# Kernel optimization log

Measured on AMD Instinct MI355X. Metric: run time of the kernel, lower is better.

Reference implementation:

```python
import jax, jax.numpy as jnp
import numpy as np

B, CL, H, W, NP = 128, 8, 16, 16, 32   # batch, primary cap length, height, width, n primary capsules
NC, CLO, ITER = 10, 16, 3              # n output capsules, output capsule length, routing iterations


def squash(t):
    # TensorMONK Activations 'squash': squash along axis 2 of a 3D tensor
    ss = jnp.sum(t * t, axis=2, keepdims=True)
    return (ss / (1.0 + ss)) * t / jnp.sqrt(ss)


def setup_inputs() -> dict:
    key = jax.random.key(0)
    k1, k2 = jax.random.split(key)
    tensor = jax.random.normal(k1, (B, CL, H, W, NP), dtype=jnp.float32)
    # nn.Parameter(torch.randn(...).normal_(0.0, 0.1)) -> N(0, 0.1)
    weight = 0.1 * jax.random.normal(k2, (CL * H * W, NP, NC * CLO), dtype=jnp.float32)
    return {"tensor": tensor, "weight": weight}


def reference(tensor, weight):
    b, cl, h, w, n_prim = tensor.shape
    # flatten spatial/length dims, squash along primary-capsule axis (dim 2, faithful to source)
    x = squash(tensor.reshape(b, -1, n_prim))                  # (B, P, N) with P = cl*h*w
    # (B,P,1,N) @ (P,N,K) broadcasted matmul -> (B,P,K)
    u = jnp.einsum('bpn,pnk->bpk', x, weight)
    u = u.reshape(b, cl, h, w, NC, CLO)                        # (B, cl, h, w, NC, CLO)
    bias = jnp.zeros((b, cl, h, w, NC), dtype=tensor.dtype)
    v = None
    for i in range(ITER):  # fixed small iteration count
        c = jax.nn.softmax(bias, axis=4)                       # softmax over output capsules
        s = jnp.einsum('bchwn,bchwnk->bnk', c, u)              # weighted sum over cl,h,w
        v = squash(s)                                          # squash along capsule length (axis 2)
        if i < ITER - 1:
            bias = bias + jnp.einsum('bchwnk,bnk->bchwn', u, v)
    return v
```

## Files before the change

### kernel.cpp

```cpp
#include <hip/hip_runtime.h>

typedef unsigned short u16;
typedef __attribute__((ext_vector_type(8))) short bf16x8;
typedef __attribute__((ext_vector_type(4))) float f32x4;

#define B_   128
#define P_   2048
#define NC_  10
#define F_   160
#define NBLK 512
#define PPB  4
#define NTHR 512
#define XS   40
#define WS   40

__device__ __forceinline__ u16 f2bf(float f) {
    union { float f; unsigned u; } v; v.f = f;
    unsigned r = v.u + 0x7FFFu + ((v.u >> 16) & 1u);
    return (u16)(r >> 16);
}
__device__ __forceinline__ float bf2f(u16 h) {
    union { unsigned u; float f; } v; v.u = ((unsigned)h) << 16;
    return v.f;
}

__global__ void k_squash_x(const float* __restrict__ t, u16* __restrict__ xb) {
    int g = blockIdx.x * 256 + threadIdx.x;
    int pair = g >> 2, sub = g & 3;
    int p = pair & 2047, b = pair >> 11;
    const float4* tg = (const float4*)t;
    int fi = pair * 8 + sub * 2;
    float4 va = tg[fi], vb = tg[fi + 1];
    float ss = va.x*va.x + va.y*va.y + va.z*va.z + va.w*va.w
             + vb.x*vb.x + vb.y*vb.y + vb.z*vb.z + vb.w*vb.w;
    ss += __shfl_xor(ss, 1);
    ss += __shfl_xor(ss, 2);
    float fct = ss / ((1.f + ss) * sqrtf(ss));
    u16 h[8] __attribute__((aligned(16)));
    h[0]=f2bf(va.x*fct); h[1]=f2bf(va.y*fct); h[2]=f2bf(va.z*fct); h[3]=f2bf(va.w*fct);
    h[4]=f2bf(vb.x*fct); h[5]=f2bf(vb.y*fct); h[6]=f2bf(vb.z*fct); h[7]=f2bf(vb.w*fct);
    *(uint4*)(xb + (p * 128 + b) * 32 + sub * 8) = *(const uint4*)h;
}

__global__ void k_wt(const float* __restrict__ w, u16* __restrict__ wb) {
    __shared__ u16 wl[32 * F_];
    int p = blockIdx.x, tid = threadIdx.x;
    const float4* wp = (const float4*)(w + p * 32 * F_);
    for (int e4 = tid; e4 < 1280; e4 += 256) {
        float4 v = wp[e4];
        u16 h[4] __attribute__((aligned(8)));
        h[0]=f2bf(v.x); h[1]=f2bf(v.y); h[2]=f2bf(v.z); h[3]=f2bf(v.w);
        *(ushort4*)(wl + e4 * 4) = *(const ushort4*)h;
    }
    __syncthreads();
    u16* wo = wb + p * F_ * 32;
    for (int sid = tid; sid < 640; sid += 256) {
        int f = sid >> 2, k0 = (sid & 3) << 3;
        u16 tmp[8] __attribute__((aligned(16)));
#pragma unroll
        for (int j = 0; j < 8; ++j) tmp[j] = wl[(k0 + j) * F_ + f];
        *(uint4*)(wo + f * 32 + k0) = *(const uint4*)tmp;
    }
}

template<int MODE>
__global__ __launch_bounds__(NTHR, 2) void k_pass(
        const u16* __restrict__ xb, const u16* __restrict__ wb,
        const float* __restrict__ vprev, u16* __restrict__ s_part)
{
    __shared__ u16 xt[128 * XS];
    __shared__ u16 wt[F_ * WS];
    const int tid = threadIdx.x, blk = blockIdx.x;
    const int L = tid & 63, wv = tid >> 6;
    const int q = L >> 4, col = L & 15;
    const int b = wv * 16 + col;
    const int p0 = blk * PPB;

    float4 vv[NC_];
    if (MODE != 0) {
#pragma unroll
        for (int n = 0; n < NC_; ++n)
            vv[n] = *(const float4*)(vprev + b * F_ + n * 16 + q * 4);
    }

    f32x4 s_acc[NC_];
#pragma unroll
    for (int n = 0; n < NC_; ++n) s_acc[n] = (f32x4){0.f, 0.f, 0.f, 0.f};

    uint4 r0, r1, r2;
    {
        const uint4* xg = (const uint4*)(xb + p0 * 4096);
        const uint4* wg = (const uint4*)(wb + p0 * 5120);
        r0 = xg[tid]; r1 = wg[tid];
        if (tid < 128) r2 = wg[tid + 512];
    }

#pragma unroll
    for (int pp = 0; pp < PPB; ++pp) {
        __syncthreads();
        *(uint4*)&xt[(tid >> 2) * XS + (tid & 3) * 8] = r0;
        *(uint4*)&wt[(tid >> 2) * WS + (tid & 3) * 8] = r1;
        if (tid < 128)
            *(uint4*)&wt[(128 + (tid >> 2)) * WS + (tid & 3) * 8] = r2;
        if (pp + 1 < PPB) {
            const uint4* xg = (const uint4*)(xb + (p0 + pp + 1) * 4096);
            const uint4* wg = (const uint4*)(wb + (p0 + pp + 1) * 5120);
            r0 = xg[tid]; r1 = wg[tid];
            if (tid < 128) r2 = wg[tid + 512];
        }
        __syncthreads();

        bf16x8 bfrag = *(const bf16x8*)&xt[b * XS + q * 8];
        if (MODE == 0) {
#pragma unroll
            for (int n = 0; n < NC_; ++n) {
                bf16x8 afrag = *(const bf16x8*)&wt[(n * 16 + col) * WS + q * 8];
                s_acc[n] = __builtin_amdgcn_mfma_f32_16x16x32_bf16(afrag, bfrag, s_acc[n], 0, 0, 0);
            }
        } else {
            float tt[NC_];
#pragma unroll
            for (int n = 0; n < NC_; ++n) {
                bf16x8 afrag = *(const bf16x8*)&wt[(n * 16 + col) * WS + q * 8];
                f32x4 z = {0.f, 0.f, 0.f, 0.f};
                f32x4 acc = __builtin_amdgcn_mfma_f32_16x16x32_bf16(afrag, bfrag, z, 0, 0, 0);
                float t = acc[0]*vv[n].x + acc[1]*vv[n].y + acc[2]*vv[n].z + acc[3]*vv[n].w;
                t += __shfl_xor(t, 16);
                t += __shfl_xor(t, 32);
                tt[n] = t;
            }
            float mx = tt[0];
#pragma unroll
            for (int n = 1; n < NC_; ++n) mx = fmaxf(mx, tt[n]);
            float den = 0.f;
#pragma unroll
            for (int n = 0; n < NC_; ++n) { tt[n] = __expf(tt[n] - mx); den += tt[n]; }
            float inv = 1.f / den;
#pragma unroll
            for (int n = 0; n < NC_; ++n) {
                bf16x8 afrag = *(const bf16x8*)&wt[(n * 16 + col) * WS + q * 8];
                f32x4 z = {0.f, 0.f, 0.f, 0.f};
                f32x4 acc = __builtin_amdgcn_mfma_f32_16x16x32_bf16(afrag, bfrag, z, 0, 0, 0);
                float cf = tt[n] * inv;
#pragma unroll
                for (int r = 0; r < 4; ++r) s_acc[n][r] += cf * acc[r];
            }
        }
    }

    u16* sp = s_part + blk * (B_ * F_);
    const float sc = (MODE == 0) ? 0.1f : 1.f;
#pragma unroll
    for (int n = 0; n < NC_; ++n) {
        u16 h[4] __attribute__((aligned(8)));
#pragma unroll
        for (int r = 0; r < 4; ++r) h[r] = f2bf(s_acc[n][r] * sc);
        *(ushort4*)(sp + b * F_ + n * 16 + q * 4) = *(const ushort4*)h;
    }
}

template<int ADD>
__global__ void k_red(const u16* __restrict__ s_part,
                      const float* __restrict__ vprev, float* __restrict__ vout) {
    __shared__ float r0s[256], r1s[256];
    const int tid = threadIdx.x, blk = blockIdx.x;
    const int pid = tid & 31, part = tid >> 5;
    const uint* sp = (const uint*)s_part;
    const int opair = blk * 32 + pid;
    float a0 = 0.f, a1 = 0.f;
#pragma unroll 8
    for (int g = part; g < NBLK; g += 8) {
        uint u = sp[g * 10240 + opair];
        a0 += bf2f((u16)(u & 0xffff));
        a1 += bf2f((u16)(u >> 16));
    }
    r0s[tid] = a0; r1s[tid] = a1;
    __syncthreads();
    if (tid < 32) {
        float s0 = 0.f, s1 = 0.f;
#pragma unroll
        for (int k = 0; k < 8; ++k) { s0 += r0s[k * 32 + tid]; s1 += r1s[k * 32 + tid]; }
        float sq = s0 * s0 + s1 * s1;
        sq += __shfl_xor(sq, 1);
        sq += __shfl_xor(sq, 2);
        sq += __shfl_xor(sq, 4);
        float fct = sq / ((1.f + sq) * sqrtf(sq));
        float2 o = make_float2(s0 * fct, s1 * fct);
        if (ADD) {
            float2 pv = *(const float2*)(vprev + 2 * (blk * 32 + tid));
            o.x += pv.x; o.y += pv.y;
        }
        *(float2*)(vout + 2 * (blk * 32 + tid)) = o;
    }
}

extern "C" void kernel_launch(void* const* d_in, const int* in_sizes, int n_in,
                              void* d_out, int out_size, void* d_ws, size_t ws_size,
                              hipStream_t stream) {
    const float* tensor = (const float*)d_in[0];
    const float* weight = (const float*)d_in[1];
    float* out = (float*)d_out;
    char* ws = (char*)d_ws;

    u16*   xb     = (u16*)(ws);
    u16*   wb     = (u16*)(ws + 16777216);
    u16*   s_part = (u16*)(ws + 37748736);
    float* v0     = (float*)(ws + 58720256);
    float* vs     = (float*)(ws + 58802176);

    k_squash_x<<<4096, 256, 0, stream>>>(tensor, xb);
    k_wt<<<2048, 256, 0, stream>>>(weight, wb);

    k_pass<0><<<NBLK, NTHR, 0, stream>>>(xb, wb, nullptr, s_part);
    k_red<0><<<320, 256, 0, stream>>>(s_part, nullptr, v0);
    k_pass<1><<<NBLK, NTHR, 0, stream>>>(xb, wb, v0, s_part);
    k_red<1><<<320, 256, 0, stream>>>(s_part, v0, vs);
    k_pass<2><<<NBLK, NTHR, 0, stream>>>(xb, wb, vs, s_part);
    k_red<0><<<320, 256, 0, stream>>>(s_part, nullptr, out);
}
```

Before: 174.1 us.

## Fuse routing passes into one cooperative kernel with LDS-resident tiles

Replaces the three pass kernels and three reduce kernels with a single cooperative kernel. Each of 256 blocks loads its 8 primary positions of x and W into shared memory once, then reuses them across all routing iterations, with grid.sync between the partial-sum and reduction phases. It also XOR-swizzles the bf16 layouts of x and W to cut LDS bank conflicts, and computes u once per position instead of running the MFMA twice in routing iterations. The cost is about 150 KB of LDS per block, which limits occupancy to one block per CU, plus grid-wide barriers. The previous multi-kernel path is kept as a fallback if the cooperative launch fails.

```diff
diff --git a/kernel.cpp b/kernel.cpp
--- a/kernel.cpp
+++ b/kernel.cpp
@@ -1,18 +1,25 @@
 #include <hip/hip_runtime.h>
+#include <hip/hip_cooperative_groups.h>
+
+namespace cg = cooperative_groups;
 
 typedef unsigned short u16;
+typedef unsigned int u32;
 typedef __attribute__((ext_vector_type(8))) short bf16x8;
 typedef __attribute__((ext_vector_type(4))) float f32x4;
 
-#define B_   128
-#define P_   2048
-#define NC_  10
-#define F_   160
-#define NBLK 512
-#define PPB  4
-#define NTHR 512
-#define XS   40
-#define WS   40
+#define B_    128
+#define P_    2048
+#define NC_   10
+#define F_    160
+#define NTHR  512
+
+#define CBLK  256
+#define CPPB  8
+
+#define GBLK  512
+#define XS    40
+#define WS    40
 
 __device__ __forceinline__ u16 f2bf(float f) {
     union { float f; unsigned u; } v; v.f = f;
@@ -39,7 +46,8 @@
     u16 h[8] __attribute__((aligned(16)));
     h[0]=f2bf(va.x*fct); h[1]=f2bf(va.y*fct); h[2]=f2bf(va.z*fct); h[3]=f2bf(va.w*fct);
     h[4]=f2bf(vb.x*fct); h[5]=f2bf(vb.y*fct); h[6]=f2bf(vb.z*fct); h[7]=f2bf(vb.w*fct);
-    *(uint4*)(xb + (p * 128 + b) * 32 + sub * 8) = *(const uint4*)h;
+    int sw = sub ^ ((b >> 1) & 3);
+    *(uint4*)(xb + (p * 128 + b) * 32 + sw * 8) = *(const uint4*)h;
 }
 
 __global__ void k_wt(const float* __restrict__ w, u16* __restrict__ wb) {
@@ -59,7 +67,160 @@
         u16 tmp[8] __attribute__((aligned(16)));
 #pragma unroll
         for (int j = 0; j < 8; ++j) tmp[j] = wl[(k0 + j) * F_ + f];
-        *(uint4*)(wo + f * 32 + k0) = *(const uint4*)tmp;
+        int sw = (sid & 3) ^ ((f >> 1) & 3);
+        *(uint4*)(wo + f * 32 + sw * 8) = *(const uint4*)tmp;
+    }
+}
+
+__global__ __launch_bounds__(NTHR, 2) void k_route(
+        const u16* __restrict__ xb, const u16* __restrict__ wb,
+        u16* __restrict__ s_part, float* __restrict__ v0,
+        float* __restrict__ vs, float* __restrict__ out)
+{
+    __shared__ u16 xt[CPPB * 128 * 32];
+    __shared__ u16 wt[CPPB * 160 * 32];
+    __shared__ float red[2 * NTHR];
+
+    const int tid = threadIdx.x, blk = blockIdx.x;
+    const int L = tid & 63, wv = tid >> 6;
+    const int q = L >> 4, col = L & 15;
+    const int b = wv * 16 + col;
+    const int qs = (q ^ ((col >> 1) & 3)) * 8;
+    const int p0 = blk * CPPB;
+
+    {
+        const uint4* xg = (const uint4*)(xb + (size_t)p0 * 4096);
+        const uint4* wg = (const uint4*)(wb + (size_t)p0 * 5120);
+        uint4 rx[8], rw[10];
+#pragma unroll
+        for (int i = 0; i < 8; ++i)  rx[i] = xg[i * NTHR + tid];
+#pragma unroll
+        for (int i = 0; i < 10; ++i) rw[i] = wg[i * NTHR + tid];
+        uint4* xl = (uint4*)xt; uint4* wl4 = (uint4*)wt;
+#pragma unroll
+        for (int i = 0; i < 8; ++i)  xl[i * NTHR + tid] = rx[i];
+#pragma unroll
+        for (int i = 0; i < 10; ++i) wl4[i * NTHR + tid] = rw[i];
+    }
+    __syncthreads();
+
+    cg::grid_group grid = cg::this_grid();
+
+    for (int itn = 0; itn < 3; ++itn) {
+        f32x4 s_acc[NC_];
+#pragma unroll
+        for (int n = 0; n < NC_; ++n) s_acc[n] = (f32x4){0.f, 0.f, 0.f, 0.f};
+
+        if (itn == 0) {
+            for (int pp = 0; pp < CPPB; ++pp) {
+                bf16x8 bfrag = *(const bf16x8*)&xt[(pp * 128 + b) * 32 + qs];
+#pragma unroll
+                for (int n = 0; n < NC_; ++n) {
+                    bf16x8 afrag = *(const bf16x8*)&wt[(pp * 160 + n * 16 + col) * 32 + qs];
+                    s_acc[n] = __builtin_amdgcn_mfma_f32_16x16x32_bf16(afrag, bfrag, s_acc[n], 0, 0, 0);
+                }
+            }
+        } else {
+            const float* vp = (itn == 1) ? v0 : vs;
+            float4 vv[NC_];
+#pragma unroll
+            for (int n = 0; n < NC_; ++n)
+                vv[n] = *(const float4*)(vp + b * F_ + n * 16 + q * 4);
+            for (int pp = 0; pp < CPPB; ++pp) {
+                bf16x8 bfrag = *(const bf16x8*)&xt[(pp * 128 + b) * 32 + qs];
+                f32x4 u[NC_];
+                float tt[NC_];
+#pragma unroll
+                for (int n = 0; n < NC_; ++n) {
+                    bf16x8 afrag = *(const bf16x8*)&wt[(pp * 160 + n * 16 + col) * 32 + qs];
+                    f32x4 z = (f32x4){0.f, 0.f, 0.f, 0.f};
+                    u[n] = __builtin_amdgcn_mfma_f32_16x16x32_bf16(afrag, bfrag, z, 0, 0, 0);
+                }
+#pragma unroll
+                for (int n = 0; n < NC_; ++n) {
+                    float t = u[n][0]*vv[n].x + u[n][1]*vv[n].y + u[n][2]*vv[n].z + u[n][3]*vv[n].w;
+                    t += __shfl_xor(t, 16);
+                    t += __shfl_xor(t, 32);
+                    tt[n] = t;
+                }
+                float mx = tt[0];
+#pragma unroll
+                for (int n = 1; n < NC_; ++n) mx = fmaxf(mx, tt[n]);
+                float den = 0.f;
+#pragma unroll
+                for (int n = 0; n < NC_; ++n) { tt[n] = __expf(tt[n] - mx); den += tt[n]; }
+                float inv = 1.f / den;
+#pragma unroll
+                for (int n = 0; n < NC_; ++n) {
+                    float cf = tt[n] * inv;
+#pragma unroll
+                    for (int r = 0; r < 4; ++r) s_acc[n][r] += cf * u[n][r];
+                }
+            }
+        }
+
+        {
+            u16* sp = s_part + blk * (B_ * F_);
+            const float sc = (itn == 0) ? 0.1f : 1.f;
+#pragma unroll
+            for (int n = 0; n < NC_; ++n) {
+                u16 h[4] __attribute__((aligned(8)));
+#pragma unroll
+                for (int r = 0; r < 4; ++r) h[r] = f2bf(s_acc[n][r] * sc);
+                *(ushort4*)(sp + b * F_ + n * 16 + q * 4) = *(const ushort4*)h;
+            }
+        }
+        __threadfence();
+        grid.sync();
+
+        {
+            const int jtid = tid & 255;
+            const int jblk = (tid < 256) ? blk : blk + CBLK;
+            const bool valid = (jblk < 320);
+            const int pid = jtid & 31, part = jtid >> 5;
+            float a0 = 0.f, a1 = 0.f;
+            if (valid) {
+                const u32* spp = (const u32*)s_part;
+                const int opair = jblk * 32 + pid;
+#pragma unroll 8
+                for (int g = part; g < CBLK; g += 8) {
+                    u32 uv = spp[g * 10240 + opair];
+                    a0 += bf2f((u16)(uv & 0xffff));
+                    a1 += bf2f((u16)(uv >> 16));
+                }
+            }
+            red[tid] = a0; red[NTHR + tid] = a1;
+            __syncthreads();
+            if (jtid < 32 && valid) {
+                const int base = (tid < 256) ? 0 : 256;
+                float s0 = 0.f, s1 = 0.f;
+#pragma unroll
+                for (int k = 0; k < 8; ++k) {
+                    s0 += red[base + k * 32 + jtid];
+                    s1 += red[NTHR + base + k * 32 + jtid];
+                }
+                float sq = s0 * s0 + s1 * s1;
+                sq += __shfl_xor(sq, 1);
+                sq += __shfl_xor(sq, 2);
+                sq += __shfl_xor(sq, 4);
+                float fct = sq / ((1.f + sq) * sqrtf(sq));
+                float ox = s0 * fct, oy = s1 * fct;
+                const int oi = 2 * (jblk * 32 + jtid);
+                if (itn == 0) {
+                    *(float2*)(v0 + oi) = make_float2(ox, oy);
+                } else if (itn == 1) {
+                    float2 pv = *(const float2*)(v0 + oi);
+                    *(float2*)(vs + oi) = make_float2(ox + pv.x, oy + pv.y);
+                } else {
+                    *(float2*)(out + oi) = make_float2(ox, oy);
+                }
+            }
+            __syncthreads();
+        }
+        if (itn < 2) {
+            __threadfence();
+            grid.sync();
+        }
     }
 }
 
@@ -74,7 +235,8 @@
     const int L = tid & 63, wv = tid >> 6;
     const int q = L >> 4, col = L & 15;
     const int b = wv * 16 + col;
-    const int p0 = blk * PPB;
+    const int qs = (q ^ ((col >> 1) & 3)) * 8;
+    const int p0 = blk * 4;
 
     float4 vv[NC_];
     if (MODE != 0) {
@@ -96,13 +258,13 @@
     }
 
 #pragma unroll
-    for (int pp = 0; pp < PPB; ++pp) {
+    for (int pp = 0; pp < 4; ++pp) {
         __syncthreads();
         *(uint4*)&xt[(tid >> 2) * XS + (tid & 3) * 8] = r0;
         *(uint4*)&wt[(tid >> 2) * WS + (tid & 3) * 8] = r1;
         if (tid < 128)
             *(uint4*)&wt[(128 + (tid >> 2)) * WS + (tid & 3) * 8] = r2;
-        if (pp + 1 < PPB) {
+        if (pp + 1 < 4) {
             const uint4* xg = (const uint4*)(xb + (p0 + pp + 1) * 4096);
             const uint4* wg = (const uint4*)(wb + (p0 + pp + 1) * 5120);
             r0 = xg[tid]; r1 = wg[tid];
@@ -110,18 +272,18 @@
         }
         __syncthreads();
 
-        bf16x8 bfrag = *(const bf16x8*)&xt[b * XS + q * 8];
+        bf16x8 bfrag = *(const bf16x8*)&xt[b * XS + qs];
         if (MODE == 0) {
 #pragma unroll
             for (int n = 0; n < NC_; ++n) {
-                bf16x8 afrag = *(const bf16x8*)&wt[(n * 16 + col) * WS + q * 8];
+                bf16x8 afrag = *(const bf16x8*)&wt[(n * 16 + col) * WS + qs];
                 s_acc[n] = __builtin_amdgcn_mfma_f32_16x16x32_bf16(afrag, bfrag, s_acc[n], 0, 0, 0);
             }
         } else {
             float tt[NC_];
 #pragma unroll
             for (int n = 0; n < NC_; ++n) {
-                bf16x8 afrag = *(const bf16x8*)&wt[(n * 16 + col) * WS + q * 8];
+                bf16x8 afrag = *(const bf16x8*)&wt[(n * 16 + col) * WS + qs];
                 f32x4 z = {0.f, 0.f, 0.f, 0.f};
                 f32x4 acc = __builtin_amdgcn_mfma_f32_16x16x32_bf16(afrag, bfrag, z, 0, 0, 0);
                 float t = acc[0]*vv[n].x + acc[1]*vv[n].y + acc[2]*vv[n].z + acc[3]*vv[n].w;
@@ -138,7 +300,7 @@
             float inv = 1.f / den;
 #pragma unroll
             for (int n = 0; n < NC_; ++n) {
-                bf16x8 afrag = *(const bf16x8*)&wt[(n * 16 + col) * WS + q * 8];
+                bf16x8 afrag = *(const bf16x8*)&wt[(n * 16 + col) * WS + qs];
                 f32x4 z = {0.f, 0.f, 0.f, 0.f};
                 f32x4 acc = __builtin_amdgcn_mfma_f32_16x16x32_bf16(afrag, bfrag, z, 0, 0, 0);
                 float cf = tt[n] * inv;
@@ -165,14 +327,14 @@
     __shared__ float r0s[256], r1s[256];
     const int tid = threadIdx.x, blk = blockIdx.x;
     const int pid = tid & 31, part = tid >> 5;
-    const uint* sp = (const uint*)s_part;
+    const u32* sp = (const u32*)s_part;
     const int opair = blk * 32 + pid;
     float a0 = 0.f, a1 = 0.f;
 #pragma unroll 8
-    for (int g = part; g < NBLK; g += 8) {
-        uint u = sp[g * 10240 + opair];
-        a0 += bf2f((u16)(u & 0xffff));
-        a1 += bf2f((u16)(u >> 16));
+    for (int g = part; g < GBLK; g += 8) {
+        u32 uv = sp[g * 10240 + opair];
+        a0 += bf2f((u16)(uv & 0xffff));
+        a1 += bf2f((u16)(uv >> 16));
     }
     r0s[tid] = a0; r1s[tid] = a1;
     __syncthreads();
@@ -211,10 +373,17 @@
     k_squash_x<<<4096, 256, 0, stream>>>(tensor, xb);
     k_wt<<<2048, 256, 0, stream>>>(weight, wb);
 
-    k_pass<0><<<NBLK, NTHR, 0, stream>>>(xb, wb, nullptr, s_part);
-    k_red<0><<<320, 256, 0, stream>>>(s_part, nullptr, v0);
-    k_pass<1><<<NBLK, NTHR, 0, stream>>>(xb, wb, v0, s_part);
-    k_red<1><<<320, 256, 0, stream>>>(s_part, v0, vs);
-    k_pass<2><<<NBLK, NTHR, 0, stream>>>(xb, wb, vs, s_part);
-    k_red<0><<<320, 256, 0, stream>>>(s_part, nullptr, out);
-}
+    void* args[6] = { (void*)&xb, (void*)&wb, (void*)&s_part,
+                      (void*)&v0, (void*)&vs, (void*)&out };
+    hipError_t err = hipLaunchCooperativeKernel((const void*)k_route, dim3(CBLK),
+                                                dim3(NTHR), args, 0, stream);
+    if (err != hipSuccess) {
+        (void)hipGetLastError();
+        k_pass<0><<<GBLK, NTHR, 0, stream>>>(xb, wb, nullptr, s_part);
+        k_red<0><<<320, 256, 0, stream>>>(s_part, nullptr, v0);
+        k_pass<1><<<GBLK, NTHR, 0, stream>>>(xb, wb, v0, s_part);
+        k_red<1><<<320, 256, 0, stream>>>(s_part, v0, vs);
+        k_pass<2><<<GBLK, NTHR, 0, stream>>>(xb, wb, vs, s_part);
+        k_red<0><<<320, 256, 0, stream>>>(s_part, nullptr, out);
+    }
+}
```

Measured after the change: 602.9 us. +246.4%, slower.
